# Kernel tuning notes

Measured on AMD Instinct MI355X. Metric: run time of the kernel, lower is better.

Reference implementation:

```python
import jax, jax.numpy as jnp
import numpy as np

N, E, G = 100000, 800000, 64
F_IN, H = 92, 4
D1, D2, D3 = 32, 64, 128  # per-head out dims: hidden//2, hidden, 2*hidden
HID, LAT = 64, 128
FINAL = H * D3  # 512
NEG_SLOPE = 0.2


def _p(key, shape, scale=0.05):
    return jax.random.normal(key, shape, dtype=jnp.float32) * scale


def setup_inputs() -> dict:
    key = jax.random.key(0)
    ks = jax.random.split(key, 32)
    node_feat = jax.random.normal(ks[0], (N, F_IN), dtype=jnp.float32)
    src = jax.random.randint(ks[1], (E,), 0, N)
    dst = jax.random.randint(ks[2], (E,), 0, N)
    graph_id = jnp.sort(jax.random.randint(ks[3], (N,), 0, G))
    d = {"node_feat": node_feat, "src": src, "dst": dst, "graph_id": graph_id}
    # GAT layer params (DGL GATConv: fc no bias, attn_l/attn_r [H,D], bias [H*D])
    dims = [(F_IN, D1), (H * D1, D2), (H * D2, D3)]
    i = 4
    for li, (fi, do) in enumerate(dims, 1):
        d[f"W{li}"] = _p(ks[i], (fi, H * do)); i += 1
        d[f"al{li}"] = _p(ks[i], (H, do)); i += 1
        d[f"ar{li}"] = _p(ks[i], (H, do)); i += 1
        d[f"b{li}"] = jnp.zeros((H * do,), dtype=jnp.float32)
    # gate MLP: Linear(final, hid) -> ReLU -> Linear(hid, 1)
    d["Wg1"] = _p(ks[i], (FINAL, HID)); i += 1
    d["bg1"] = jnp.zeros((HID,), dtype=jnp.float32)
    d["Wg2"] = _p(ks[i], (HID, 1)); i += 1
    d["bg2"] = jnp.zeros((1,), dtype=jnp.float32)
    d["Wmu"] = _p(ks[i], (FINAL, LAT)); i += 1
    d["bmu"] = jnp.zeros((LAT,), dtype=jnp.float32)
    d["Wlv"] = _p(ks[i], (FINAL, LAT)); i += 1
    d["blv"] = jnp.zeros((LAT,), dtype=jnp.float32)
    return d


def gat_layer(h, W, al, ar, b, src, dst, heads, d_out):
    n = h.shape[0]
    Wh = (h @ W).reshape(n, heads, d_out)                      # [N,H,D]
    el = jnp.einsum('nhd,hd->nh', Wh, al)                      # a_l . Wh
    er = jnp.einsum('nhd,hd->nh', Wh, ar)
    e = jax.nn.leaky_relu(el[src] + er[dst], NEG_SLOPE)        # [E,H]
    m = jax.ops.segment_max(e, dst, num_segments=n)
    m = jnp.where(jnp.isfinite(m), m, 0.0)                     # zero-in-degree guard
    ex = jnp.exp(e - m[dst])
    s = jax.ops.segment_sum(ex, dst, num_segments=n)
    a = ex / jnp.maximum(s[dst], 1e-9)                         # edge softmax
    msg = a[:, :, None] * Wh[src]                              # [E,H,D] (peak intermediate)
    out = jax.ops.segment_sum(msg, dst, num_segments=n)        # scatter-aggregate
    out = out + b.reshape(1, heads, d_out)
    return out.reshape(n, heads * d_out)                       # flatten(1)


def attention_pool(h, graph_id, Wg1, bg1, Wg2, bg2, num_graphs):
    gate = jax.nn.relu(h @ Wg1 + bg1) @ Wg2 + bg2              # [N,1]
    m = jax.ops.segment_max(gate, graph_id, num_segments=num_graphs)
    ex = jnp.exp(gate - m[graph_id])
    s = jax.ops.segment_sum(ex, graph_id, num_segments=num_graphs)
    a = ex / jnp.maximum(s[graph_id], 1e-9)                    # softmax over nodes per graph
    return jax.ops.segment_sum(a * h, graph_id, num_segments=num_graphs)  # [G,final]


def reference(node_feat, src, dst, graph_id,
              W1, al1, ar1, b1, W2, al2, ar2, b2, W3, al3, ar3, b3,
              Wg1, bg1, Wg2, bg2, Wmu, bmu, Wlv, blv):
    h = jax.nn.elu(gat_layer(node_feat, W1, al1, ar1, b1, src, dst, H, D1))
    h = jax.nn.elu(gat_layer(h, W2, al2, ar2, b2, src, dst, H, D2))
    h = jax.nn.elu(gat_layer(h, W3, al3, ar3, b3, src, dst, H, D3))
    g = attention_pool(h, graph_id, Wg1, bg1, Wg2, bg2, G)
    mu = g @ Wmu + bmu
    logvar = g @ Wlv + blv
    return (mu, logvar)
```

## Files before the change

### kernel.cpp

```cpp
#include <hip/hip_runtime.h>
#include <math.h>

#define NNODES 100000
#define NEDGES 800000
#define NGRAPH 64
#define NHEAD  4
#define FINALD 512
#define HIDG   64
#define LATD   128
#define K1P    96
#define NB_SCAN 98
#define PQ     16

typedef unsigned int uint;
typedef unsigned short ushort;
typedef __attribute__((ext_vector_type(8))) short bf16x8;
typedef __attribute__((ext_vector_type(4))) float f32x4;

__device__ __forceinline__ float bflo(uint u) { return __uint_as_float(u << 16); }
__device__ __forceinline__ float bfhi(uint u) { return __uint_as_float(u & 0xffff0000u); }
__device__ __forceinline__ ushort f2bf(float f) {
    uint u = __float_as_uint(f);
    return (ushort)((u + 0x7fffu + ((u >> 16) & 1u)) >> 16);
}
__device__ __forceinline__ uint pack2(float a, float b) {
    return (uint)f2bf(a) | ((uint)f2bf(b) << 16);
}
__device__ __forceinline__ void fmabf2(float w, uint v, float& a0, float& a1) {
    a0 = fmaf(w, bflo(v), a0);
    a1 = fmaf(w, bfhi(v), a1);
}

__device__ __forceinline__ void async_copy16(const ushort* gsrc, ushort* lds_base) {
    __builtin_amdgcn_global_load_lds(
        (const __attribute__((address_space(1))) uint*)gsrc,
        (__attribute__((address_space(3))) uint*)lds_base,
        16, 0, 0);
}

__global__ void count_kernel(const int* __restrict__ dst, int* __restrict__ deg) {
    int e = blockIdx.x * blockDim.x + threadIdx.x;
    if (e < NEDGES) atomicAdd(&deg[dst[e]], 1);
}
__global__ __launch_bounds__(1024) void scan_block_kernel(const int* __restrict__ deg,
                                                          int* __restrict__ off,
                                                          int* __restrict__ bsum) {
    __shared__ int buf[1024];
    int t = threadIdx.x;
    int i = blockIdx.x * 1024 + t;
    int x = (i < NNODES) ? deg[i] : 0;
    buf[t] = x;
    __syncthreads();
    for (int s = 1; s < 1024; s <<= 1) {
        int v = (t >= s) ? buf[t - s] : 0;
        __syncthreads();
        buf[t] += v;
        __syncthreads();
    }
    if (i < NNODES) off[i] = buf[t] - x;
    if (t == 1023) bsum[blockIdx.x] = buf[1023];
}
__global__ __launch_bounds__(128) void scan_bsum_kernel(int* __restrict__ bsum) {
    __shared__ int buf[128];
    int t = threadIdx.x;
    int x = (t < NB_SCAN) ? bsum[t] : 0;
    buf[t] = x;
    __syncthreads();
    for (int s = 1; s < 128; s <<= 1) {
        int v = (t >= s) ? buf[t - s] : 0;
        __syncthreads();
        buf[t] += v;
        __syncthreads();
    }
    if (t < NB_SCAN) bsum[t] = buf[t] - x;
    if (t == 0) bsum[NB_SCAN] = buf[NB_SCAN - 1];
}
__global__ __launch_bounds__(1024) void scan_add_kernel(int* __restrict__ off,
                                                        const int* __restrict__ bsum,
                                                        int* __restrict__ cursor) {
    int i = blockIdx.x * 1024 + threadIdx.x;
    if (i < NNODES) {
        int v = off[i] + bsum[blockIdx.x];
        off[i] = v;
        cursor[i] = v;
    }
    if (i == 0) off[NNODES] = bsum[NB_SCAN];
}
__global__ void scatter_kernel(const int* __restrict__ src, const int* __restrict__ dst,
                               int* __restrict__ cursor, int* __restrict__ src_csr) {
    int e = blockIdx.x * blockDim.x + threadIdx.x;
    if (e >= NEDGES) return;
    int p = atomicAdd(&cursor[dst[e]], 1);
    src_csr[p] = src[e];
}

#define C1 (128 * K1P)
#define C2 (256 * 128)
#define C3 (512 * 256)
#define CG (64 * 512)
#define CX (NNODES * K1P)
#define CTOT (C1 + C2 + C3 + CG + CX + NNODES + NNODES + NGRAPH + 1)
__global__ void conv_all_kernel(const float* __restrict__ W1, const float* __restrict__ W2,
                                const float* __restrict__ W3, const float* __restrict__ Wg1,
                                const float* __restrict__ nf,
                                ushort* __restrict__ Bt1, ushort* __restrict__ Bt2,
                                ushort* __restrict__ Bt3, ushort* __restrict__ Btg,
                                ushort* __restrict__ x0, float* __restrict__ gate,
                                int* __restrict__ deg, const int* __restrict__ gid,
                                int* __restrict__ gstart) {
    int i = blockIdx.x * blockDim.x + threadIdx.x;
    if (i < C1) {
        int n = i / K1P, k = i - n * K1P;
        Bt1[i] = (k < 92) ? f2bf(W1[(size_t)k * 128 + n]) : (ushort)0;
        return;
    }
    i -= C1;
    if (i < C2) {
        int n = i >> 7, k = i & 127;
        Bt2[i] = f2bf(W2[(size_t)k * 256 + n]);
        return;
    }
    i -= C2;
    if (i < C3) {
        int n = i >> 8, k = i & 255;
        Bt3[i] = f2bf(W3[(size_t)k * 512 + n]);
        return;
    }
    i -= C3;
    if (i < CG) {
        int n = i >> 9, k = i & 511;
        Btg[i] = f2bf(Wg1[(size_t)k * 64 + n]);
        return;
    }
    i -= CG;
    if (i < CX) {
        int n = i / K1P, k = i - n * K1P;
        x0[i] = (k < 92) ? f2bf(nf[(size_t)n * 92 + k]) : (ushort)0;
        return;
    }
    i -= CX;
    if (i < NNODES) { gate[i] = 0.f; return; }
    i -= NNODES;
    if (i < NNODES) { deg[i] = 0; return; }
    i -= NNODES;
    if (i <= NGRAPH) {
        int lo = 0, hi = NNODES;
        while (lo < hi) {
            int mid = (lo + hi) >> 1;
            if (gid[mid] < i) lo = mid + 1; else hi = mid;
        }
        gstart[i] = lo;
    }
}

template <int BN, int MODE>
__global__ __launch_bounds__(256) void mfma_gemm(const ushort* __restrict__ A,
                                                 const ushort* __restrict__ Bt,
                                                 const float* __restrict__ bias,
                                                 ushort* __restrict__ C,
                                                 const float* __restrict__ Wg2,
                                                 float* __restrict__ gate,
                                                 int M, int K, int N) {
    constexpr int WNS = BN / 2;
    constexpr int NT = WNS / 16;
    __shared__ ushort Alds[128][32];
    __shared__ ushort Blds[BN][32];
    int tid = threadIdx.x;
    int wave = tid >> 6, lane = tid & 63;
    int wm = wave & 1, wn = wave >> 1;
    int quad = lane >> 4, l16 = lane & 15;
    int rowBase = blockIdx.y * 128;
    int colBase = blockIdx.x * BN;

    int srow = lane >> 2;
    int scol = (lane & 3) * 8;

    f32x4 acc[4][NT];
#pragma unroll
    for (int i = 0; i < 4; i++)
#pragma unroll
        for (int j = 0; j < NT; j++) acc[i][j] = (f32x4){0.f, 0.f, 0.f, 0.f};

    for (int k0 = 0; k0 < K; k0 += 32) {
#pragma unroll
        for (int c = 0; c < 2; c++) {
            int chunk = wave * 2 + c;
            int row = rowBase + chunk * 16 + srow;
            async_copy16(&A[(size_t)row * K + k0 + scol], &Alds[chunk * 16][0]);
        }
        if constexpr (BN == 128) {
#pragma unroll
            for (int c = 0; c < 2; c++) {
                int chunk = wave * 2 + c;
                int row = colBase + chunk * 16 + srow;
                async_copy16(&Bt[(size_t)row * K + k0 + scol], &Blds[chunk * 16][0]);
            }
        } else {
            int row = colBase + wave * 16 + srow;
            async_copy16(&Bt[(size_t)row * K + k0 + scol], &Blds[wave * 16][0]);
        }
        __syncthreads();
        bf16x8 af[4], bf[NT];
#pragma unroll
        for (int i = 0; i < 4; i++)
            af[i] = *(const bf16x8*)&Alds[wm * 64 + i * 16 + l16][quad * 8];
#pragma unroll
        for (int j = 0; j < NT; j++)
            bf[j] = *(const bf16x8*)&Blds[wn * WNS + j * 16 + l16][quad * 8];
#pragma unroll
        for (int i = 0; i < 4; i++)
#pragma unroll
            for (int j = 0; j < NT; j++)
                acc[i][j] = __builtin_amdgcn_mfma_f32_16x16x32_bf16(af[i], bf[j], acc[i][j], 0, 0, 0);
        __syncthreads();
    }

    if constexpr (MODE == 0) {
#pragma unroll
        for (int i = 0; i < 4; i++) {
#pragma unroll
            for (int j = 0; j < NT; j++) {
                int col = colBase + wn * WNS + j * 16 + l16;
#pragma unroll
                for (int r = 0; r < 4; r++) {
                    int row = rowBase + wm * 64 + i * 16 + quad * 4 + r;
                    if (row < M) C[(size_t)row * N + col] = f2bf(acc[i][j][r]);
                }
            }
        }
    } else {
        float bb[NT], wg[NT];
#pragma unroll
        for (int j = 0; j < NT; j++) {
            int col = colBase + wn * WNS + j * 16 + l16;
            bb[j] = bias[col];
            wg[j] = Wg2[col];
        }
#pragma unroll
        for (int i = 0; i < 4; i++) {
            float pd[4] = {0.f, 0.f, 0.f, 0.f};
#pragma unroll
            for (int j = 0; j < NT; j++) {
#pragma unroll
                for (int r = 0; r < 4; r++) {
                    float x = fmaxf(acc[i][j][r] + bb[j], 0.f);
                    pd[r] = fmaf(x, wg[j], pd[r]);
                }
            }
#pragma unroll
            for (int m = 1; m < 16; m <<= 1)
#pragma unroll
                for (int r = 0; r < 4; r++)
                    pd[r] += __shfl_xor(pd[r], m, 64);
            if (l16 == 0) {
#pragma unroll
                for (int r = 0; r < 4; r++) {
                    int row = rowBase + wm * 64 + i * 16 + quad * 4 + r;
                    if (row < M) atomicAdd(&gate[row], pd[r]);
                }
            }
        }
    }
}

template <int HD>
__global__ __launch_bounds__(256) void eler_node(const ushort* __restrict__ Wh,
                                                 const float* __restrict__ al,
                                                 const float* __restrict__ ar,
                                                 float* __restrict__ el,
                                                 float* __restrict__ er) {
    constexpr int LPN = HD / 8;
    constexpr int NPW = 64 / LPN;
    constexpr int S = (HD / NHEAD) / 8;
    int wave = threadIdx.x >> 6;
    int lane = threadIdx.x & 63;
    int sub = lane & (LPN - 1);
    int n = blockIdx.x * (4 * NPW) + wave * NPW + lane / LPN;
    int d0 = sub * 8;
    uint4 v = *(const uint4*)&Wh[(size_t)n * HD + d0];
    float w0 = bflo(v.x), w1 = bfhi(v.x), w2 = bflo(v.y), w3 = bfhi(v.y);
    float w4 = bflo(v.z), w5 = bfhi(v.z), w6 = bflo(v.w), w7 = bfhi(v.w);
    float4 a0 = *(const float4*)&al[d0];
    float4 a1 = *(const float4*)&al[d0 + 4];
    float4 b0 = *(const float4*)&ar[d0];
    float4 b1 = *(const float4*)&ar[d0 + 4];
    float sl, sr;
    sl = w0 * a0.x; sl = fmaf(w1, a0.y, sl); sl = fmaf(w2, a0.z, sl); sl = fmaf(w3, a0.w, sl);
    sl = fmaf(w4, a1.x, sl); sl = fmaf(w5, a1.y, sl); sl = fmaf(w6, a1.z, sl); sl = fmaf(w7, a1.w, sl);
    sr = w0 * b0.x; sr = fmaf(w1, b0.y, sr); sr = fmaf(w2, b0.z, sr); sr = fmaf(w3, b0.w, sr);
    sr = fmaf(w4, b1.x, sr); sr = fmaf(w5, b1.y, sr); sr = fmaf(w6, b1.z, sr); sr = fmaf(w7, b1.w, sr);
#pragma unroll
    for (int o = S / 2; o > 0; o >>= 1) {
        sl += __shfl_down(sl, o, 64);
        sr += __shfl_down(sr, o, 64);
    }
    if ((sub & (S - 1)) == 0) {
        int h = sub / S;
        el[n * 4 + h] = sl;
        er[n * 4 + h] = sr;
    }
}

__global__ void attn_node(const int* __restrict__ src_csr, const int* __restrict__ off,
                          const float4* __restrict__ el4, const float4* __restrict__ er4,
                          float4* __restrict__ aw4, float4* __restrict__ nsum4) {
    int n = blockIdx.x * blockDim.x + threadIdx.x;
    if (n >= NNODES) return;
    int i0 = off[n], i1 = off[n + 1];
    float4 ern = er4[n];
    float4 s = make_float4(0.f, 0.f, 0.f, 0.f);
    for (int i = i0; i < i1; i += 8) {
        int cnt = i1 - i; if (cnt > 8) cnt = 8;
        int s8[8];
#pragma unroll
        for (int j = 0; j < 8; j++)
            if (j < cnt) s8[j] = src_csr[i + j];
        float4 e8[8];
#pragma unroll
        for (int j = 0; j < 8; j++)
            if (j < cnt) e8[j] = el4[s8[j]];
#pragma unroll
        for (int j = 0; j < 8; j++) {
            if (j < cnt) {
                float4 x = e8[j];
                x.x += ern.x; x.y += ern.y; x.z += ern.z; x.w += ern.w;
                x.x = (x.x >= 0.f) ? x.x : 0.2f * x.x;
                x.y = (x.y >= 0.f) ? x.y : 0.2f * x.y;
                x.z = (x.z >= 0.f) ? x.z : 0.2f * x.z;
                x.w = (x.w >= 0.f) ? x.w : 0.2f * x.w;
                x.x = expf(x.x - 8.f); x.y = expf(x.y - 8.f);
                x.z = expf(x.z - 8.f); x.w = expf(x.w - 8.f);
                aw4[i + j] = x;
                s.x += x.x; s.y += x.y; s.z += x.z; s.w += x.w;
            }
        }
    }
    nsum4[n] = s;
}

template <int HD, int DPL>
__global__ __launch_bounds__(256) void gat_aggregate2(const int* __restrict__ src_csr,
                                                      const int* __restrict__ off,
                                                      const ushort* __restrict__ Wh,
                                                      const float* __restrict__ aw,
                                                      const float* __restrict__ nsum,
                                                      const float* __restrict__ bias,
                                                      ushort* __restrict__ out,
                                                      int pass) {
    constexpr int LOGD = (HD == 128) ? 5 : (HD == 256) ? 6 : 7;
    const int lane = threadIdx.x & 63;
    const int wv = __builtin_amdgcn_readfirstlane((int)(threadIdx.x >> 6));
    const int n = blockIdx.x * 4 + wv;
    const int d = pass * (64 * DPL) + lane * DPL;
    const int h = d >> LOGD;
    const int i0 = __builtin_amdgcn_readfirstlane(off[n]);
    const int i1 = __builtin_amdgcn_readfirstlane(off[n + 1]);

    float a0 = 0.f, a1 = 0.f, a2 = 0.f, a3 = 0.f;
    const ushort* __restrict__ col = Wh + d;

    int i = i0;
    for (; i + 4 <= i1; i += 4) {
        const int s0 = __builtin_amdgcn_readfirstlane(src_csr[i + 0]);
        const int s1 = __builtin_amdgcn_readfirstlane(src_csr[i + 1]);
        const int s2 = __builtin_amdgcn_readfirstlane(src_csr[i + 2]);
        const int s3 = __builtin_amdgcn_readfirstlane(src_csr[i + 3]);
        const float w0 = aw[(i + 0) * 4 + h];
        const float w1 = aw[(i + 1) * 4 + h];
        const float w2 = aw[(i + 2) * 4 + h];
        const float w3 = aw[(i + 3) * 4 + h];
        if constexpr (DPL == 4) {
            uint2 v0 = *(const uint2*)&col[(size_t)s0 * HD];
            uint2 v1 = *(const uint2*)&col[(size_t)s1 * HD];
            uint2 v2 = *(const uint2*)&col[(size_t)s2 * HD];
            uint2 v3 = *(const uint2*)&col[(size_t)s3 * HD];
            fmabf2(w0, v0.x, a0, a1); fmabf2(w0, v0.y, a2, a3);
            fmabf2(w1, v1.x, a0, a1); fmabf2(w1, v1.y, a2, a3);
            fmabf2(w2, v2.x, a0, a1); fmabf2(w2, v2.y, a2, a3);
            fmabf2(w3, v3.x, a0, a1); fmabf2(w3, v3.y, a2, a3);
        } else {
            uint v0 = *(const uint*)&col[(size_t)s0 * HD];
            uint v1 = *(const uint*)&col[(size_t)s1 * HD];
            uint v2 = *(const uint*)&col[(size_t)s2 * HD];
            uint v3 = *(const uint*)&col[(size_t)s3 * HD];
            fmabf2(w0, v0, a0, a1);
            fmabf2(w1, v1, a0, a1);
            fmabf2(w2, v2, a0, a1);
            fmabf2(w3, v3, a0, a1);
        }
    }
    for (; i < i1; ++i) {
        const int s0 = __builtin_amdgcn_readfirstlane(src_csr[i]);
        const float w0 = aw[i * 4 + h];
        if constexpr (DPL == 4) {
            uint2 v0 = *(const uint2*)&col[(size_t)s0 * HD];
            fmabf2(w0, v0.x, a0, a1); fmabf2(w0, v0.y, a2, a3);
        } else {
            uint v0 = *(const uint*)&col[(size_t)s0 * HD];
            fmabf2(w0, v0, a0, a1);
        }
    }

    const float inv = 1.f / fmaxf(nsum[n * 4 + h], 1e-9f);
    float x0 = a0 * inv + bias[d + 0];
    float x1 = a1 * inv + bias[d + 1];
    x0 = (x0 > 0.f) ? x0 : (expf(x0) - 1.f);
    x1 = (x1 > 0.f) ? x1 : (expf(x1) - 1.f);
    if constexpr (DPL == 4) {
        float x2 = a2 * inv + bias[d + 2];
        float x3 = a3 * inv + bias[d + 3];
        x2 = (x2 > 0.f) ? x2 : (expf(x2) - 1.f);
        x3 = (x3 > 0.f) ? x3 : (expf(x3) - 1.f);
        uint2 o;
        o.x = pack2(x0, x1);
        o.y = pack2(x2, x3);
        *(uint2*)&out[(size_t)n * HD + d] = o;
    } else {
        *(uint*)&out[(size_t)n * HD + d] = pack2(x0, x1);
    }
}

__global__ __launch_bounds__(128) void pool_partial(const ushort* __restrict__ h,
                                                    const float* __restrict__ gate,
                                                    const int* __restrict__ gstart,
                                                    float* __restrict__ partial) {
    int g = blockIdx.x, q = blockIdx.y;
    int n0 = gstart[g], n1 = gstart[g + 1];
    __shared__ float red[128];
    int t = threadIdx.x;
    float m = -1e30f;
    for (int n = n0 + t; n < n1; n += 128) m = fmaxf(m, gate[n]);
    red[t] = m; __syncthreads();
    for (int s = 64; s > 0; s >>= 1) {
        if (t < s) red[t] = fmaxf(red[t], red[t + s]);
        __syncthreads();
    }
    m = red[0];

    int len = n1 - n0;
    int chunk = (len + PQ - 1) / PQ;
    int s = n0 + q * chunk;
    int e = s + chunk; if (e > n1) e = n1;
    int d4 = t;
    const uint2* h2 = (const uint2*)h;
    float a0 = 0.f, a1 = 0.f, a2 = 0.f, a3 = 0.f;
    for (int n = s; n < e; n++) {
        float w = expf(gate[n] - m);
        uint2 v = h2[(size_t)n * 128 + d4];
        a0 = fmaf(w, bflo(v.x), a0);
        a1 = fmaf(w, bfhi(v.x), a1);
        a2 = fmaf(w, bflo(v.y), a2);
        a3 = fmaf(w, bfhi(v.y), a3);
    }
    *(float4*)&partial[((size_t)(g * PQ + q)) * FINALD + d4 * 4] = make_float4(a0, a1, a2, a3);
}

__global__ __launch_bounds__(128) void final_kernel(const float* __restrict__ partial,
                                                    const float* __restrict__ gate,
                                                    const int* __restrict__ gstart,
                                                    const float* __restrict__ Wmu,
                                                    const float* __restrict__ bmu,
                                                    const float* __restrict__ Wlv,
                                                    const float* __restrict__ blv,
                                                    float* __restrict__ out) {
    int g = blockIdx.x, j = threadIdx.x;
    int n0 = gstart[g], n1 = gstart[g + 1];
    __shared__ float red[128];
    __shared__ float pooled[FINALD];
    float m = -1e30f;
    for (int n = n0 + j; n < n1; n += 128) m = fmaxf(m, gate[n]);
    red[j] = m; __syncthreads();
    for (int s = 64; s > 0; s >>= 1) {
        if (j < s) red[j] = fmaxf(red[j], red[j + s]);
        __syncthreads();
    }
    m = red[0]; __syncthreads();
    float sum = 0.f;
    for (int n = n0 + j; n < n1; n += 128) sum += expf(gate[n] - m);
    red[j] = sum; __syncthreads();
    for (int s = 64; s > 0; s >>= 1) {
        if (j < s) red[j] += red[j + s];
        __syncthreads();
    }
    float gsum = red[0];

    const float* p = partial + (size_t)g * PQ * FINALD;
    for (int k = j; k < FINALD; k += 128) {
        float v = 0.f;
#pragma unroll
        for (int q = 0; q < PQ; q++) v += p[q * FINALD + k];
        pooled[k] = v;
    }
    __syncthreads();
    float am = 0.f, av = 0.f;
    for (int k = 0; k < FINALD; k++) {
        float pv = pooled[k];
        am = fmaf(pv, Wmu[k * LATD + j], am);
        av = fmaf(pv, Wlv[k * LATD + j], av);
    }
    float inv = 1.f / fmaxf(gsum, 1e-9f);
    out[g * LATD + j] = am * inv + bmu[j];
    out[NGRAPH * LATD + g * LATD + j] = av * inv + blv[j];
}

extern "C" void kernel_launch(void* const* d_in, const int* in_sizes, int n_in,
                              void* d_out, int out_size, void* d_ws, size_t ws_size,
                              hipStream_t stream) {
    (void)in_sizes; (void)n_in; (void)out_size; (void)ws_size;
    const float* node_feat = (const float*)d_in[0];
    const int* src = (const int*)d_in[1];
    const int* dst = (const int*)d_in[2];
    const int* gid = (const int*)d_in[3];
    const float* W[3]    = {(const float*)d_in[4],  (const float*)d_in[8],  (const float*)d_in[12]};
    const float* al[3]   = {(const float*)d_in[5],  (const float*)d_in[9],  (const float*)d_in[13]};
    const float* ar[3]   = {(const float*)d_in[6],  (const float*)d_in[10], (const float*)d_in[14]};
    const float* bias[3] = {(const float*)d_in[7],  (const float*)d_in[11], (const float*)d_in[15]};
    const float* Wg1 = (const float*)d_in[16];
    const float* bg1 = (const float*)d_in[17];
    const float* Wg2 = (const float*)d_in[18];
    const float* Wmu = (const float*)d_in[20];
    const float* bmu = (const float*)d_in[21];
    const float* Wlv = (const float*)d_in[22];
    const float* blv = (const float*)d_in[23];

    char* ws = (char*)d_ws;
    size_t woff = 0;
    auto carve = [&](size_t bytes) {
        void* p = ws + woff;
        woff = (woff + bytes + 255) & ~(size_t)255;
        return p;
    };
    ushort* hA      = (ushort*)carve((size_t)NNODES * 512 * 2);
    ushort* hB      = (ushort*)carve((size_t)NNODES * 512 * 2);
    float*  el      = (float*) carve((size_t)NNODES * 4 * 4);
    float*  er      = (float*) carve((size_t)NNODES * 4 * 4);
    float*  aw      = (float*) carve((size_t)NEDGES * 4 * 4);
    float*  nsum    = (float*) carve((size_t)NNODES * 4 * 4);
    int*    deg     = (int*)   carve((size_t)NNODES * 4);
    int*    off     = (int*)   carve((size_t)(NNODES + 1) * 4);
    int*    cursor  = (int*)   carve((size_t)NNODES * 4);
    int*    src_csr = (int*)   carve((size_t)NEDGES * 4);
    int*    bsum    = (int*)   carve((size_t)(NB_SCAN + 1) * 4);
    float*  gate    = (float*) carve((size_t)NNODES * 4);
    int*    gstart  = (int*)   carve((size_t)(NGRAPH + 1) * 4);
    float*  partial = (float*) carve((size_t)NGRAPH * PQ * FINALD * 4);
    ushort* Bt1     = (ushort*)carve((size_t)128 * K1P * 2);
    ushort* Bt2     = (ushort*)carve((size_t)256 * 128 * 2);
    ushort* Bt3     = (ushort*)carve((size_t)512 * 256 * 2);
    ushort* Btg     = (ushort*)carve((size_t)64 * 512 * 2 + 4096);
    ushort* x0      = hA;

    conv_all_kernel<<<(CTOT + 255) / 256, 256, 0, stream>>>(
        W[0], W[1], W[2], Wg1, node_feat, Bt1, Bt2, Bt3, Btg, x0, gate, deg, gid, gstart);
    count_kernel<<<(NEDGES + 255) / 256, 256, 0, stream>>>(dst, deg);
    scan_block_kernel<<<NB_SCAN, 1024, 0, stream>>>(deg, off, bsum);
    scan_bsum_kernel<<<1, 128, 0, stream>>>(bsum);
    scan_add_kernel<<<NB_SCAN, 1024, 0, stream>>>(off, bsum, cursor);
    scatter_kernel<<<(NEDGES + 255) / 256, 256, 0, stream>>>(src, dst, cursor, src_csr);

    const int MB = (NNODES + 127) / 128;
    const int AGB = NNODES / 4;

    mfma_gemm<128, 0><<<dim3(1, MB), 256, 0, stream>>>(
        x0, Bt1, nullptr, hB, nullptr, nullptr, NNODES, K1P, 128);
    eler_node<128><<<NNODES / 16, 256, 0, stream>>>(hB, al[0], ar[0], el, er);
    attn_node<<<(NNODES + 255) / 256, 256, 0, stream>>>(
        src_csr, off, (const float4*)el, (const float4*)er, (float4*)aw, (float4*)nsum);
    gat_aggregate2<128, 2><<<AGB, 256, 0, stream>>>(
        src_csr, off, hB, aw, nsum, bias[0], hA, 0);

    mfma_gemm<128, 0><<<dim3(2, MB), 256, 0, stream>>>(
        hA, Bt2, nullptr, hB, nullptr, nullptr, NNODES, 128, 256);
    eler_node<256><<<NNODES / 8, 256, 0, stream>>>(hB, al[1], ar[1], el, er);
    attn_node<<<(NNODES + 255) / 256, 256, 0, stream>>>(
        src_csr, off, (const float4*)el, (const float4*)er, (float4*)aw, (float4*)nsum);
    gat_aggregate2<256, 4><<<AGB, 256, 0, stream>>>(
        src_csr, off, hB, aw, nsum, bias[1], hA, 0);

    mfma_gemm<128, 0><<<dim3(4, MB), 256, 0, stream>>>(
        hA, Bt3, nullptr, hB, nullptr, nullptr, NNODES, 256, 512);
    eler_node<512><<<NNODES / 4, 256, 0, stream>>>(hB, al[2], ar[2], el, er);
    attn_node<<<(NNODES + 255) / 256, 256, 0, stream>>>(
        src_csr, off, (const float4*)el, (const float4*)er, (float4*)aw, (float4*)nsum);
    gat_aggregate2<512, 4><<<AGB, 256, 0, stream>>>(
        src_csr, off, hB, aw, nsum, bias[2], hA, 0);
    gat_aggregate2<512, 4><<<AGB, 256, 0, stream>>>(
        src_csr, off, hB, aw, nsum, bias[2], hA, 1);

    mfma_gemm<64, 1><<<dim3(1, MB), 256, 0, stream>>>(
        hA, Btg, bg1, nullptr, Wg2, gate, NNODES, FINALD, HIDG);
    pool_partial<<<dim3(NGRAPH, PQ), 128, 0, stream>>>(hA, gate, gstart, partial);
    final_kernel<<<NGRAPH, 128, 0, stream>>>(partial, gate, gstart, Wmu, bmu, Wlv, blv, (float*)d_out);
}
```

Before: 739.7 us.

## Compute attention weights per edge and fold softmax sum into aggregation

Replaces the per-node attention kernel, which loops serially over in-edges, with a per-edge kernel so work is balanced across threads regardless of degree. It adds a dst_csr array written during the CSR scatter so each edge can look up its destination's er. The per-node softmax denominator is no longer stored; gat_aggregate2 accumulates it from the edge weights it already reads. The cost is an extra 3.2MB index array and some redundant summing in the aggregation lanes.

```diff
diff --git a/kernel.cpp b/kernel.cpp
--- a/kernel.cpp
+++ b/kernel.cpp
@@ -87,11 +87,14 @@
     if (i == 0) off[NNODES] = bsum[NB_SCAN];
 }
 __global__ void scatter_kernel(const int* __restrict__ src, const int* __restrict__ dst,
-                               int* __restrict__ cursor, int* __restrict__ src_csr) {
+                               int* __restrict__ cursor, int* __restrict__ src_csr,
+                               int* __restrict__ dst_csr) {
     int e = blockIdx.x * blockDim.x + threadIdx.x;
     if (e >= NEDGES) return;
-    int p = atomicAdd(&cursor[dst[e]], 1);
+    int d = dst[e];
+    int p = atomicAdd(&cursor[d], 1);
     src_csr[p] = src[e];
+    dst_csr[p] = d;
 }
 
 #define C1 (128 * K1P)
@@ -301,41 +304,24 @@
     }
 }
 
-__global__ void attn_node(const int* __restrict__ src_csr, const int* __restrict__ off,
+__global__ void attn_edge(const int* __restrict__ src_csr, const int* __restrict__ dst_csr,
                           const float4* __restrict__ el4, const float4* __restrict__ er4,
-                          float4* __restrict__ aw4, float4* __restrict__ nsum4) {
-    int n = blockIdx.x * blockDim.x + threadIdx.x;
-    if (n >= NNODES) return;
-    int i0 = off[n], i1 = off[n + 1];
-    float4 ern = er4[n];
-    float4 s = make_float4(0.f, 0.f, 0.f, 0.f);
-    for (int i = i0; i < i1; i += 8) {
-        int cnt = i1 - i; if (cnt > 8) cnt = 8;
-        int s8[8];
-#pragma unroll
-        for (int j = 0; j < 8; j++)
-            if (j < cnt) s8[j] = src_csr[i + j];
-        float4 e8[8];
-#pragma unroll
-        for (int j = 0; j < 8; j++)
-            if (j < cnt) e8[j] = el4[s8[j]];
-#pragma unroll
-        for (int j = 0; j < 8; j++) {
-            if (j < cnt) {
-                float4 x = e8[j];
-                x.x += ern.x; x.y += ern.y; x.z += ern.z; x.w += ern.w;
-                x.x = (x.x >= 0.f) ? x.x : 0.2f * x.x;
-                x.y = (x.y >= 0.f) ? x.y : 0.2f * x.y;
-                x.z = (x.z >= 0.f) ? x.z : 0.2f * x.z;
-                x.w = (x.w >= 0.f) ? x.w : 0.2f * x.w;
-                x.x = expf(x.x - 8.f); x.y = expf(x.y - 8.f);
-                x.z = expf(x.z - 8.f); x.w = expf(x.w - 8.f);
-                aw4[i + j] = x;
-                s.x += x.x; s.y += x.y; s.z += x.z; s.w += x.w;
-            }
-        }
-    }
-    nsum4[n] = s;
+                          float4* __restrict__ aw4) {
+    int i = blockIdx.x * blockDim.x + threadIdx.x;
+    if (i >= NEDGES) return;
+    int s = src_csr[i];
+    int d = dst_csr[i];
+    float4 a = el4[s];
+    float4 b = er4[d];
+    float x0 = a.x + b.x, x1 = a.y + b.y, x2 = a.z + b.z, x3 = a.w + b.w;
+    x0 = (x0 >= 0.f) ? x0 : 0.2f * x0;
+    x1 = (x1 >= 0.f) ? x1 : 0.2f * x1;
+    x2 = (x2 >= 0.f) ? x2 : 0.2f * x2;
+    x3 = (x3 >= 0.f) ? x3 : 0.2f * x3;
+    float4 w;
+    w.x = expf(x0 - 8.f); w.y = expf(x1 - 8.f);
+    w.z = expf(x2 - 8.f); w.w = expf(x3 - 8.f);
+    aw4[i] = w;
 }
 
 template <int HD, int DPL>
@@ -343,7 +329,6 @@
                                                       const int* __restrict__ off,
                                                       const ushort* __restrict__ Wh,
                                                       const float* __restrict__ aw,
-                                                      const float* __restrict__ nsum,
                                                       const float* __restrict__ bias,
                                                       ushort* __restrict__ out,
                                                       int pass) {
@@ -357,6 +342,7 @@
     const int i1 = __builtin_amdgcn_readfirstlane(off[n + 1]);
 
     float a0 = 0.f, a1 = 0.f, a2 = 0.f, a3 = 0.f;
+    float ssum = 0.f;
     const ushort* __restrict__ col = Wh + d;
 
     int i = i0;
@@ -369,6 +355,7 @@
         const float w1 = aw[(i + 1) * 4 + h];
         const float w2 = aw[(i + 2) * 4 + h];
         const float w3 = aw[(i + 3) * 4 + h];
+        ssum += w0; ssum += w1; ssum += w2; ssum += w3;
         if constexpr (DPL == 4) {
             uint2 v0 = *(const uint2*)&col[(size_t)s0 * HD];
             uint2 v1 = *(const uint2*)&col[(size_t)s1 * HD];
@@ -392,6 +379,7 @@
     for (; i < i1; ++i) {
         const int s0 = __builtin_amdgcn_readfirstlane(src_csr[i]);
         const float w0 = aw[i * 4 + h];
+        ssum += w0;
         if constexpr (DPL == 4) {
             uint2 v0 = *(const uint2*)&col[(size_t)s0 * HD];
             fmabf2(w0, v0.x, a0, a1); fmabf2(w0, v0.y, a2, a3);
@@ -401,7 +389,7 @@
         }
     }
 
-    const float inv = 1.f / fmaxf(nsum[n * 4 + h], 1e-9f);
+    const float inv = 1.f / fmaxf(ssum, 1e-9f);
     float x0 = a0 * inv + bias[d + 0];
     float x1 = a1 * inv + bias[d + 1];
     x0 = (x0 > 0.f) ? x0 : (expf(x0) - 1.f);
@@ -535,11 +523,11 @@
     float*  el      = (float*) carve((size_t)NNODES * 4 * 4);
     float*  er      = (float*) carve((size_t)NNODES * 4 * 4);
     float*  aw      = (float*) carve((size_t)NEDGES * 4 * 4);
-    float*  nsum    = (float*) carve((size_t)NNODES * 4 * 4);
     int*    deg     = (int*)   carve((size_t)NNODES * 4);
     int*    off     = (int*)   carve((size_t)(NNODES + 1) * 4);
     int*    cursor  = (int*)   carve((size_t)NNODES * 4);
     int*    src_csr = (int*)   carve((size_t)NEDGES * 4);
+    int*    dst_csr = (int*)   carve((size_t)NEDGES * 4);
     int*    bsum    = (int*)   carve((size_t)(NB_SCAN + 1) * 4);
     float*  gate    = (float*) carve((size_t)NNODES * 4);
     int*    gstart  = (int*)   carve((size_t)(NGRAPH + 1) * 4);
@@ -556,36 +544,37 @@
     scan_block_kernel<<<NB_SCAN, 1024, 0, stream>>>(deg, off, bsum);
     scan_bsum_kernel<<<1, 128, 0, stream>>>(bsum);
     scan_add_kernel<<<NB_SCAN, 1024, 0, stream>>>(off, bsum, cursor);
-    scatter_kernel<<<(NEDGES + 255) / 256, 256, 0, stream>>>(src, dst, cursor, src_csr);
+    scatter_kernel<<<(NEDGES + 255) / 256, 256, 0, stream>>>(src, dst, cursor, src_csr, dst_csr);
 
     const int MB = (NNODES + 127) / 128;
     const int AGB = NNODES / 4;
+    const int EB = (NEDGES + 255) / 256;
 
     mfma_gemm<128, 0><<<dim3(1, MB), 256, 0, stream>>>(
         x0, Bt1, nullptr, hB, nullptr, nullptr, NNODES, K1P, 128);
     eler_node<128><<<NNODES / 16, 256, 0, stream>>>(hB, al[0], ar[0], el, er);
-    attn_node<<<(NNODES + 255) / 256, 256, 0, stream>>>(
-        src_csr, off, (const float4*)el, (const float4*)er, (float4*)aw, (float4*)nsum);
+    attn_edge<<<EB, 256, 0, stream>>>(
+        src_csr, dst_csr, (const float4*)el, (const float4*)er, (float4*)aw);
     gat_aggregate2<128, 2><<<AGB, 256, 0, stream>>>(
-        src_csr, off, hB, aw, nsum, bias[0], hA, 0);
+        src_csr, off, hB, aw, bias[0], hA, 0);
 
     mfma_gemm<128, 0><<<dim3(2, MB), 256, 0, stream>>>(
         hA, Bt2, nullptr, hB, nullptr, nullptr, NNODES, 128, 256);
     eler_node<256><<<NNODES / 8, 256, 0, stream>>>(hB, al[1], ar[1], el, er);
-    attn_node<<<(NNODES + 255) / 256, 256, 0, stream>>>(
-        src_csr, off, (const float4*)el, (const float4*)er, (float4*)aw, (float4*)nsum);
+    attn_edge<<<EB, 256, 0, stream>>>(
+        src_csr, dst_csr, (const float4*)el, (const float4*)er, (float4*)aw);
     gat_aggregate2<256, 4><<<AGB, 256, 0, stream>>>(
-        src_csr, off, hB, aw, nsum, bias[1], hA, 0);
+        src_csr, off, hB, aw, bias[1], hA, 0);
 
     mfma_gemm<128, 0><<<dim3(4, MB), 256, 0, stream>>>(
         hA, Bt3, nullptr, hB, nullptr, nullptr, NNODES, 256, 512);
     eler_node<512><<<NNODES / 4, 256, 0, stream>>>(hB, al[2], ar[2], el, er);
-    attn_node<<<(NNODES + 255) / 256, 256, 0, stream>>>(
-        src_csr, off, (const float4*)el, (const float4*)er, (float4*)aw, (float4*)nsum);
+    attn_edge<<<EB, 256, 0, stream>>>(
+        src_csr, dst_csr, (const float4*)el, (const float4*)er, (float4*)aw);
     gat_aggregate2<512, 4><<<AGB, 256, 0, stream>>>(
-        src_csr, off, hB, aw, nsum, bias[2], hA, 0);
+        src_csr, off, hB, aw, bias[2], hA, 0);
     gat_aggregate2<512, 4><<<AGB, 256, 0, stream>>>(
-        src_csr, off, hB, aw, nsum, bias[2], hA, 1);
+        src_csr, off, hB, aw, bias[2], hA, 1);
 
     mfma_gemm<64, 1><<<dim3(1, MB), 256, 0, stream>>>(
         hA, Btg, bg1, nullptr, Wg2, gate, NNODES, FINALD, HIDG);
```

Result: faster. 720.0 us (-2.7%).
